# Kernel tuning notes

Hardware: AMD Instinct MI355X
Metric: run time of the kernel (lower is better)

## Reference

```python
import jax, jax.numpy as jnp
import numpy as np

N = 50000
E = 800000
D_IN = 128
H = 128
D_OUT = 64
BN_EPS = 1e-5


def setup_inputs() -> dict:
    key = jax.random.key(0)
    ks = jax.random.split(key, 20)

    def lin(k, fin, fout):
        kw, kb = jax.random.split(k)
        w = jax.random.normal(kw, (fin, fout), jnp.float32) / np.sqrt(fin)
        b = jnp.zeros((fout,), jnp.float32)
        return w, b

    def bn_params(k, d):
        kg, kb = jax.random.split(k)
        g = 1.0 + 0.1 * jax.random.normal(kg, (d,), jnp.float32)
        b = 0.1 * jax.random.normal(kb, (d,), jnp.float32)
        rm = 0.1 * jax.random.normal(jax.random.fold_in(k, 7), (d,), jnp.float32)
        rv = jnp.abs(1.0 + 0.1 * jax.random.normal(jax.random.fold_in(k, 9), (d,), jnp.float32))
        return g, b, rm, rv

    x = jax.random.normal(ks[0], (N, D_IN), jnp.float32)
    edge_index = jax.random.randint(ks[1], (2, E), 0, N, jnp.int64)
    ricci_curvature = jax.random.normal(ks[2], (E,), jnp.float32)

    W1, b1 = lin(ks[3], D_IN, H)
    Wc0, bc0 = lin(ks[4], H, H)          # convs[0]: hidden*1 -> hidden
    Wc1, bc1 = lin(ks[5], 2 * H, H)      # convs[1]: hidden*2 -> hidden
    Wout, bout = lin(ks[6], 3 * H, D_OUT)  # conv2: hidden*(L-1) -> out

    bn1_g, bn1_b, bn1_rm, bn1_rv = bn_params(ks[7], D_IN)
    bnc0_g, bnc0_b, bnc0_rm, bnc0_rv = bn_params(ks[8], H)
    bnc1_g, bnc1_b, bnc1_rm, bnc1_rv = bn_params(ks[9], 2 * H)
    bn2_g, bn2_b, bn2_rm, bn2_rv = bn_params(ks[10], 3 * H)

    return {
        "x": x, "edge_index": edge_index, "percent": 50,
        "ricci_curvature": ricci_curvature,
        "W1": W1, "b1": b1, "Wc0": Wc0, "bc0": bc0,
        "Wc1": Wc1, "bc1": bc1, "Wout": Wout, "bout": bout,
        "bn1_g": bn1_g, "bn1_b": bn1_b, "bn1_rm": bn1_rm, "bn1_rv": bn1_rv,
        "bnc0_g": bnc0_g, "bnc0_b": bnc0_b, "bnc0_rm": bnc0_rm, "bnc0_rv": bnc0_rv,
        "bnc1_g": bnc1_g, "bnc1_b": bnc1_b, "bnc1_rm": bnc1_rm, "bnc1_rv": bnc1_rv,
        "bn2_g": bn2_g, "bn2_b": bn2_b, "bn2_rm": bn2_rm, "bn2_rv": bn2_rv,
    }


def _bn_eval(h, g, b, rm, rv):
    # BatchNorm1d in eval mode: affine normalize with running stats.
    return (h - rm) * (g * jax.lax.rsqrt(rv + BN_EPS)) + b


def reference(x, edge_index, percent, ricci_curvature,
              W1, b1, Wc0, bc0, Wc1, bc1, Wout, bout,
              bn1_g, bn1_b, bn1_rm, bn1_rv,
              bnc0_g, bnc0_b, bnc0_rm, bnc0_rv,
              bnc1_g, bnc1_b, bnc1_rm, bnc1_rv,
              bn2_g, bn2_b, bn2_rm, bn2_rv):
    n = x.shape[0]
    # GCN normalization with self-loops (PyG GCNConv default), shared by all layers
    loops = jnp.arange(n, dtype=edge_index.dtype)
    row = jnp.concatenate([edge_index[0], loops])  # source
    col = jnp.concatenate([edge_index[1], loops])  # target
    deg = jax.ops.segment_sum(jnp.ones_like(col, dtype=x.dtype), col, num_segments=n)
    dinv = jax.lax.rsqrt(deg)  # deg >= 1 thanks to self loops
    norm = (dinv[row] * dinv[col])[:, None]  # [E+N, 1]

    def gcn(h, W, b):
        hw = h @ W                                   # transform first (PyG order)
        msg = hw[row] * norm                          # gather + scale per edge
        return jax.ops.segment_sum(msg, col, num_segments=n) + b

    # eval mode: no sampling / dynamic reweighting, dropout = identity
    h = _bn_eval(x, bn1_g, bn1_b, bn1_rm, bn1_rv)
    h = jax.nn.relu(gcn(h, W1, b1))
    r0 = h

    h = _bn_eval(h, bnc0_g, bnc0_b, bnc0_rm, bnc0_rv)
    h = jax.nn.relu(gcn(h, Wc0, bc0))
    r1 = h
    h = jnp.concatenate([r0, r1], axis=1)  # [N, 2H]

    h = _bn_eval(h, bnc1_g, bnc1_b, bnc1_rm, bnc1_rv)
    h = jax.nn.relu(gcn(h, Wc1, bc1))
    r2 = h
    h = jnp.concatenate([r0, r1, r2], axis=1)  # [N, 3H]

    h = _bn_eval(h, bn2_g, bn2_b, bn2_rm, bn2_rv)
    out = gcn(h, Wout, bout)
    return (out, r0, r1, r2)
```

## Files before the change

### kernel.cpp

```cpp
#include <hip/hip_runtime.h>
#include <hip/hip_bf16.h>
#include <stdint.h>

#define NN 50000
#define NE 800000

typedef unsigned short ushort8 __attribute__((ext_vector_type(8)));
typedef __bf16 bf16x8 __attribute__((ext_vector_type(8)));
typedef float f32x4 __attribute__((ext_vector_type(4)));

__device__ __forceinline__ float bf2f_bits(unsigned short u) {
  unsigned int x = ((unsigned int)u) << 16;
  float f;
  __builtin_memcpy(&f, &x, 4);
  return f;
}
__device__ __forceinline__ unsigned short f2bf_bits(float f) {
  unsigned int x;
  __builtin_memcpy(&x, &f, 4);
  unsigned int lsb = (x >> 16) & 1u;
  x += 0x7fffu + lsb;
  return (unsigned short)(x >> 16);
}
__device__ __forceinline__ float lo16(unsigned int v) { return bf2f_bits((unsigned short)v); }
__device__ __forceinline__ float hi16(unsigned int v) { return bf2f_bits((unsigned short)(v >> 16)); }
__device__ __forceinline__ float loadf(const void* base, size_t idx, int isbf) {
  if (isbf) return bf2f_bits(((const unsigned short*)base)[idx]);
  return ((const float*)base)[idx];
}

__global__ void k_sniff(const void* x, const void* ei, int* flags, int* cnt8) {
  int i = blockIdx.x * 256 + threadIdx.x;
  if (i < 8 * NN) cnt8[i] = 0;
  if (blockIdx.x != 0) return;
  __shared__ int badbf;
  __shared__ int zodd;
  int tid = threadIdx.x;
  if (tid == 0) { badbf = 0; zodd = 0; }
  __syncthreads();
  unsigned short u = ((const unsigned short*)x)[tid];
  float v = bf2f_bits(u);
  float av = fabsf(v);
  int ok = (av == 0.0f) || (av > 1e-8f && av < 1e8f);
  if (!ok) atomicAdd(&badbf, 1);
  int e32 = ((const int*)ei)[tid];
  if ((tid & 1) && e32 == 0) atomicAdd(&zodd, 1);
  __syncthreads();
  if (tid == 0) {
    flags[0] = (badbf <= 12) ? 1 : 0;
    flags[1] = (zodd >= 100) ? 1 : 0;
  }
}

__global__ void k_cvt_edges(const void* ei, int* erow, int* ecol, int* rank,
                            int* cnt8, const int* flags) {
  int e = blockIdx.x * 256 + threadIdx.x;
  if (e >= NE) return;
  unsigned int xcc;
  asm volatile("s_getreg_b32 %0, hwreg(HW_REG_XCC_ID)" : "=s"(xcc));
  xcc &= 7;
  int r, c;
  if (flags[1]) {
    const long long* p = (const long long*)ei;
    r = (int)p[e];
    c = (int)p[NE + e];
  } else {
    const int* p = (const int*)ei;
    r = p[e];
    c = p[NE + e];
  }
  erow[e] = r;
  ecol[e] = c;
  int rl = atomicAdd(&cnt8[xcc * NN + c], 1);
  rank[e] = rl | (int)(xcc << 27);
}

__global__ void k_cvt_xb(const void* x, unsigned short* xb, const int* flags) {
  if (flags[0]) return;
  int i4 = (blockIdx.x * 256 + threadIdx.x) * 4;
  if (i4 >= NN * 128) return;
  float4 v = *reinterpret_cast<const float4*>((const float*)x + i4);
  xb[i4 + 0] = f2bf_bits(v.x); xb[i4 + 1] = f2bf_bits(v.y);
  xb[i4 + 2] = f2bf_bits(v.z); xb[i4 + 3] = f2bf_bits(v.w);
}

__global__ void k_scan1(int* cnt8, int* indptr, int* bsum, float* dinv, int n) {
  __shared__ int sm[256];
  int tid = threadIdx.x;
  int i = blockIdx.x * 256 + tid;
  int v = 0;
  if (i < n) {
    int run = 0;
#pragma unroll
    for (int s = 0; s < 8; ++s) {
      int cs = cnt8[s * NN + i];
      cnt8[s * NN + i] = run;
      run += cs;
    }
    v = run;
    dinv[i] = rsqrtf((float)(v + 1));
  }
  sm[tid] = v;
  __syncthreads();
  for (int off = 1; off < 256; off <<= 1) {
    int t = (tid >= off) ? sm[tid - off] : 0;
    __syncthreads();
    sm[tid] += t;
    __syncthreads();
  }
  if (i < n) indptr[i] = sm[tid] - v;
  if (tid == 255) bsum[blockIdx.x] = sm[255];
}
__global__ void k_scan2(int* bsum, int nb) {
  __shared__ int sm[256];
  int tid = threadIdx.x;
  int v = (tid < nb) ? bsum[tid] : 0;
  sm[tid] = v;
  __syncthreads();
  for (int off = 1; off < 256; off <<= 1) {
    int t = (tid >= off) ? sm[tid - off] : 0;
    __syncthreads();
    sm[tid] += t;
    __syncthreads();
  }
  if (tid < nb) bsum[tid] = sm[tid] - v;
  if (tid == 0) bsum[nb] = sm[255];
}
__global__ void k_scan3(int* indptr, const int* bsum, int n, int nb) {
  int i = blockIdx.x * 256 + threadIdx.x;
  if (i < n) indptr[i] += bsum[i >> 8];
  else if (i == n) indptr[n] = bsum[nb];
}
__global__ void k_fill(const int* erow, const int* ecol, const int* rank,
                       const int* indptr, const int* cnt8, int* srcs) {
  int e = blockIdx.x * 256 + threadIdx.x;
  if (e >= NE) return;
  int c = ecol[e];
  int rk = rank[e];
  int sh = (unsigned int)rk >> 27;
  srcs[indptr[c] + cnt8[sh * NN + c] + (rk & 0x07FFFFFF)] = erow[e];
}

__global__ void k_prep_wt_all(
    const void* W1, const void* Wc0, const void* Wc1, const void* Wout,
    const void* g1, const void* g2, const void* g3, const void* g4,
    const void* rv1, const void* rv2, const void* rv3, const void* rv4,
    unsigned short* Wtb, const int* flags) {
  int idx = blockIdx.x * 256 + threadIdx.x;
  if (idx >= 90112) return;
  int isbf = flags[0];
  const void *W, *g, *rv;
  int K, NOUT, base;
  if (idx < 16384)      { W = W1;   g = g1; rv = rv1; K = 128; NOUT = 128; base = 0; }
  else if (idx < 32768) { W = Wc0;  g = g2; rv = rv2; K = 128; NOUT = 128; base = 16384; }
  else if (idx < 65536) { W = Wc1;  g = g3; rv = rv3; K = 256; NOUT = 128; base = 32768; }
  else                  { W = Wout; g = g4; rv = rv4; K = 384; NOUT = 64;  base = 65536; }
  int li = idx - base;
  int j = li / K, k = li % K;
  float s = loadf(g, k, isbf) * rsqrtf(loadf(rv, k, isbf) + 1e-5f);
  Wtb[idx] = f2bf_bits(s * loadf(W, (size_t)k * NOUT + j, isbf));
}
__global__ void k_prep_c_all(
    const void* W1, const void* Wc0, const void* Wc1, const void* Wout,
    const void* g1, const void* g2, const void* g3, const void* g4,
    const void* b1, const void* b2, const void* b3, const void* b4,
    const void* rm1, const void* rm2, const void* rm3, const void* rm4,
    const void* rv1, const void* rv2, const void* rv3, const void* rv4,
    float* cvec, const int* flags) {
  int jj = blockIdx.x;
  int lane = threadIdx.x;
  int isbf = flags[0];
  const void *W, *g, *bb, *rm, *rv;
  int K, NOUT, j;
  if (jj < 128)      { W = W1;   g = g1; bb = b1; rm = rm1; rv = rv1; K = 128; NOUT = 128; j = jj; }
  else if (jj < 256) { W = Wc0;  g = g2; bb = b2; rm = rm2; rv = rv2; K = 128; NOUT = 128; j = jj - 128; }
  else if (jj < 384) { W = Wc1;  g = g3; bb = b3; rm = rm3; rv = rv3; K = 256; NOUT = 128; j = jj - 256; }
  else               { W = Wout; g = g4; bb = b4; rm = rm4; rv = rv4; K = 384; NOUT = 64;  j = jj - 384; }
  float acc = 0.f;
  for (int k = lane; k < K; k += 64) {
    float s = loadf(g, k, isbf) * rsqrtf(loadf(rv, k, isbf) + 1e-5f);
    float t = loadf(bb, k, isbf) - loadf(rm, k, isbf) * s;
    acc += t * loadf(W, (size_t)k * NOUT + j, isbf);
  }
#pragma unroll
  for (int off = 32; off; off >>= 1) acc += __shfl_down(acc, off);
  if (lane == 0) cvec[jj] = acc;
}

template <int NOUT, int K>
__global__ __launch_bounds__(256) void k_gemm_mfma(
    const unsigned short* __restrict__ h0b, const unsigned short* __restrict__ h1b,
    const unsigned short* __restrict__ h2b,
    const unsigned short* __restrict__ h0d, const unsigned short* __restrict__ h1d,
    const unsigned short* __restrict__ h2d,
    const unsigned short* __restrict__ Wtb,
    const float* __restrict__ cvec, const float* __restrict__ dinv,
    unsigned short* __restrict__ hb, const int* __restrict__ flags) {
  constexpr int KS = K / 32;
  constexpr int NT = NOUT / 16;
  int isbf = flags[0];
  const unsigned short* h0 = (isbf && h0d) ? h0d : h0b;
  const unsigned short* h1 = (isbf && h1d) ? h1d : h1b;
  const unsigned short* h2 = (isbf && h2d) ? h2d : h2b;
  int tid = threadIdx.x;
  int wv = tid >> 6, lane = tid & 63;
  int row0 = blockIdx.x * 64 + wv * 16;
  int l15 = lane & 15;
  int kq = lane >> 4;
  int arow = row0 + l15;
  bool inb = arow < NN;

  bf16x8 afrag[KS];
#pragma unroll
  for (int ks = 0; ks < KS; ++ks) {
    int kg = ks * 32 + kq * 8;
    const unsigned short* src = (kg >> 7) == 0 ? h0 : ((kg >> 7) == 1 ? h1 : h2);
    ushort8 u = (ushort8)0;
    if (inb) u = *reinterpret_cast<const ushort8*>(src + (size_t)arow * 128 + (kg & 127));
    afrag[ks] = __builtin_bit_cast(bf16x8, u);
  }

  f32x4 acc[NT];
#pragma unroll
  for (int nt = 0; nt < NT; ++nt) acc[nt] = (f32x4)0.f;

#pragma unroll
  for (int nt = 0; nt < NT; ++nt) {
    const unsigned short* wrow = Wtb + (size_t)(nt * 16 + l15) * K + kq * 8;
#pragma unroll
    for (int ks = 0; ks < KS; ++ks) {
      ushort8 u = *reinterpret_cast<const ushort8*>(wrow + ks * 32);
      acc[nt] = __builtin_amdgcn_mfma_f32_16x16x32_bf16(
          afrag[ks], __builtin_bit_cast(bf16x8, u), acc[nt], 0, 0, 0);
    }
  }

  int orow0 = row0 + kq * 4;
  float dv[4];
  bool ob[4];
#pragma unroll
  for (int r = 0; r < 4; ++r) {
    int orow = orow0 + r;
    ob[r] = orow < NN;
    dv[r] = ob[r] ? dinv[orow] : 0.f;
  }
#pragma unroll
  for (int nt = 0; nt < NT; ++nt) {
    int col = nt * 16 + l15;
    float cv = cvec[col];
#pragma unroll
    for (int r = 0; r < 4; ++r) {
      if (ob[r])
        hb[(size_t)(orow0 + r) * NOUT + col] = f2bf_bits(dv[r] * (acc[nt][r] + cv));
    }
  }
}

template <bool RELU>
__global__ __launch_bounds__(256) void k_agg128(
    const unsigned short* __restrict__ hb, const int* __restrict__ indptr,
    const int* __restrict__ srcs, const float* __restrict__ dinv,
    const void* __restrict__ bias, void* __restrict__ dout, size_t region_off,
    unsigned short* __restrict__ rb, const int* __restrict__ flags) {
  int gw = __builtin_amdgcn_readfirstlane(blockIdx.x * 4 + (threadIdx.x >> 6));
  int lane = threadIdx.x & 63;
  if (gw >= NN) return;
  int isbf = flags[0];
  int e0 = indptr[gw], e1 = indptr[gw + 1];
  size_t co = (size_t)lane * 2;
  unsigned int sv = *reinterpret_cast<const unsigned int*>(hb + (size_t)gw * 128 + co);
  float a0 = lo16(sv), a1 = hi16(sv);
  float b0 = 0.f, b1 = 0.f, c0 = 0.f, c1 = 0.f, d0 = 0.f, d1 = 0.f;
  int e = e0;
  for (; e + 7 < e1; e += 8) {
    int s0 = srcs[e], s1 = srcs[e + 1], s2 = srcs[e + 2], s3 = srcs[e + 3];
    int s4 = srcs[e + 4], s5 = srcs[e + 5], s6 = srcs[e + 6], s7 = srcs[e + 7];
    unsigned int v0 = *reinterpret_cast<const unsigned int*>(hb + (size_t)s0 * 128 + co);
    unsigned int v1 = *reinterpret_cast<const unsigned int*>(hb + (size_t)s1 * 128 + co);
    unsigned int v2 = *reinterpret_cast<const unsigned int*>(hb + (size_t)s2 * 128 + co);
    unsigned int v3 = *reinterpret_cast<const unsigned int*>(hb + (size_t)s3 * 128 + co);
    unsigned int v4 = *reinterpret_cast<const unsigned int*>(hb + (size_t)s4 * 128 + co);
    unsigned int v5 = *reinterpret_cast<const unsigned int*>(hb + (size_t)s5 * 128 + co);
    unsigned int v6 = *reinterpret_cast<const unsigned int*>(hb + (size_t)s6 * 128 + co);
    unsigned int v7 = *reinterpret_cast<const unsigned int*>(hb + (size_t)s7 * 128 + co);
    a0 += lo16(v0); a1 += hi16(v0); b0 += lo16(v1); b1 += hi16(v1);
    c0 += lo16(v2); c1 += hi16(v2); d0 += lo16(v3); d1 += hi16(v3);
    a0 += lo16(v4); a1 += hi16(v4); b0 += lo16(v5); b1 += hi16(v5);
    c0 += lo16(v6); c1 += hi16(v6); d0 += lo16(v7); d1 += hi16(v7);
  }
  for (; e < e1; ++e) {
    int s0 = srcs[e];
    unsigned int v0 = *reinterpret_cast<const unsigned int*>(hb + (size_t)s0 * 128 + co);
    a0 += lo16(v0); a1 += hi16(v0);
  }
  float dv = dinv[gw];
  float o0 = dv * ((a0 + b0) + (c0 + d0)) + loadf(bias, co + 0, isbf);
  float o1 = dv * ((a1 + b1) + (c1 + d1)) + loadf(bias, co + 1, isbf);
  if (RELU) { o0 = fmaxf(o0, 0.f); o1 = fmaxf(o1, 0.f); }
  size_t eo = region_off + (size_t)gw * 128 + co;
  if (isbf) {
    unsigned int pk = (unsigned int)f2bf_bits(o0) | ((unsigned int)f2bf_bits(o1) << 16);
    *reinterpret_cast<unsigned int*>((unsigned short*)dout + eo) = pk;
  } else {
    float2 fo; fo.x = o0; fo.y = o1;
    *reinterpret_cast<float2*>((float*)dout + eo) = fo;
    unsigned int pk = (unsigned int)f2bf_bits(o0) | ((unsigned int)f2bf_bits(o1) << 16);
    *reinterpret_cast<unsigned int*>(rb + (size_t)gw * 128 + co) = pk;
  }
}

__global__ __launch_bounds__(256) void k_agg64out(
    const unsigned short* __restrict__ hb, const int* __restrict__ indptr,
    const int* __restrict__ srcs, const float* __restrict__ dinv,
    const void* __restrict__ bias, void* __restrict__ dout,
    const int* __restrict__ flags) {
  int gw = blockIdx.x * 8 + (threadIdx.x >> 5);
  int lane = threadIdx.x & 31;
  if (gw >= NN) return;
  int isbf = flags[0];
  int e0 = indptr[gw], e1 = indptr[gw + 1];
  int e = e0;
  size_t co = (size_t)lane * 2;
  unsigned int sv = *reinterpret_cast<const unsigned int*>(hb + (size_t)gw * 64 + co);
  float a0 = lo16(sv), a1 = hi16(sv);
  float b0 = 0.f, b1 = 0.f, c0 = 0.f, c1 = 0.f, d0 = 0.f, d1 = 0.f;
  for (; e + 3 < e1; e += 4) {
    int sa = srcs[e], sb = srcs[e + 1], sc = srcs[e + 2], sd = srcs[e + 3];
    unsigned int va = *reinterpret_cast<const unsigned int*>(hb + (size_t)sa * 64 + co);
    unsigned int vb = *reinterpret_cast<const unsigned int*>(hb + (size_t)sb * 64 + co);
    unsigned int vc = *reinterpret_cast<const unsigned int*>(hb + (size_t)sc * 64 + co);
    unsigned int vd = *reinterpret_cast<const unsigned int*>(hb + (size_t)sd * 64 + co);
    a0 += lo16(va); a1 += hi16(va); b0 += lo16(vb); b1 += hi16(vb);
    c0 += lo16(vc); c1 += hi16(vc); d0 += lo16(vd); d1 += hi16(vd);
  }
  for (; e < e1; ++e) {
    int sa = srcs[e];
    unsigned int va = *reinterpret_cast<const unsigned int*>(hb + (size_t)sa * 64 + co);
    a0 += lo16(va); a1 += hi16(va);
  }
  float dv = dinv[gw];
  float o0 = dv * ((a0 + b0) + (c0 + d0)) + loadf(bias, co + 0, isbf);
  float o1 = dv * ((a1 + b1) + (c1 + d1)) + loadf(bias, co + 1, isbf);
  size_t eo = (size_t)gw * 64 + co;
  if (isbf) {
    unsigned int pk = (unsigned int)f2bf_bits(o0) | ((unsigned int)f2bf_bits(o1) << 16);
    *reinterpret_cast<unsigned int*>((unsigned short*)dout + eo) = pk;
  } else {
    float2 fo; fo.x = o0; fo.y = o1;
    *reinterpret_cast<float2*>((float*)dout + eo) = fo;
  }
}

extern "C" void kernel_launch(void* const* d_in, const int* in_sizes, int n_in,
                              void* d_out, int out_size, void* d_ws, size_t ws_size,
                              hipStream_t stream) {
  const void* x    = d_in[0];
  const void* ei   = d_in[1];
  const void* W1   = d_in[4];
  const void* b1   = d_in[5];
  const void* Wc0  = d_in[6];
  const void* bc0  = d_in[7];
  const void* Wc1  = d_in[8];
  const void* bc1  = d_in[9];
  const void* Wout = d_in[10];
  const void* bout = d_in[11];
  const void *bn1g = d_in[12], *bn1b = d_in[13], *bn1rm = d_in[14], *bn1rv = d_in[15];
  const void *bc0g = d_in[16], *bc0b = d_in[17], *bc0rm = d_in[18], *bc0rv = d_in[19];
  const void *bc1g = d_in[20], *bc1b = d_in[21], *bc1rm = d_in[22], *bc1rv = d_in[23];
  const void *bn2g = d_in[24], *bn2b = d_in[25], *bn2rm = d_in[26], *bn2rv = d_in[27];
  (void)in_sizes; (void)n_in; (void)out_size; (void)ws_size;

  char* w = (char*)d_ws;
  auto carve = [&](size_t bytes) {
    char* p = w;
    w += (bytes + 255) & ~(size_t)255;
    return p;
  };
  int*   flags  = (int*)  carve(256);
  float* dinv   = (float*)carve(sizeof(float) * NN);
  int*   cnt8   = (int*)  carve(sizeof(int) * 8 * NN);
  int*   indptr = (int*)  carve(sizeof(int) * (NN + 1));
  int*   bsum   = (int*)  carve(sizeof(int) * 256);
  int*   erow   = (int*)  carve(sizeof(int) * NE);
  int*   ecol   = (int*)  carve(sizeof(int) * NE);
  int*   rank   = (int*)  carve(sizeof(int) * NE);
  int*   srcs   = (int*)  carve(sizeof(int) * NE);
  unsigned short* Wtb = (unsigned short*)carve(sizeof(short) * 90112);
  float* cvec   = (float*)carve(sizeof(float) * 448);
  unsigned short* xb  = (unsigned short*)carve(sizeof(short) * (size_t)NN * 128);
  unsigned short* hb  = (unsigned short*)carve(sizeof(short) * (size_t)NN * 128);
  unsigned short* rb0 = (unsigned short*)carve(sizeof(short) * (size_t)NN * 128);
  unsigned short* rb1 = (unsigned short*)carve(sizeof(short) * (size_t)NN * 128);
  unsigned short* rb2 = (unsigned short*)carve(sizeof(short) * (size_t)NN * 128);

  const int gN8 = (8 * NN + 255) / 256;
  const int gE = (NE + 255) / 256;
  const int nb = (NN + 255) / 256;
  const int gG = (NN + 63) / 64;
  const int gA2 = (NN + 3) / 4;
  const int gA1 = (NN + 7) / 8;

  k_sniff<<<gN8, 256, 0, stream>>>(x, ei, flags, cnt8);
  k_cvt_edges<<<gE, 256, 0, stream>>>(ei, erow, ecol, rank, cnt8, flags);
  k_cvt_xb<<<(NN * 128 / 4 + 255) / 256, 256, 0, stream>>>(x, xb, flags);
  k_scan1<<<nb, 256, 0, stream>>>(cnt8, indptr, bsum, dinv, NN);
  k_scan2<<<1, 256, 0, stream>>>(bsum, nb);
  k_scan3<<<(NN + 1 + 255) / 256, 256, 0, stream>>>(indptr, bsum, NN, nb);
  k_fill<<<gE, 256, 0, stream>>>(erow, ecol, rank, indptr, cnt8, srcs);
  k_prep_wt_all<<<(90112 + 255) / 256, 256, 0, stream>>>(
      W1, Wc0, Wc1, Wout, bn1g, bc0g, bc1g, bn2g, bn1rv, bc0rv, bc1rv, bn2rv, Wtb, flags);
  k_prep_c_all<<<448, 64, 0, stream>>>(
      W1, Wc0, Wc1, Wout, bn1g, bc0g, bc1g, bn2g, bn1b, bc0b, bc1b, bn2b,
      bn1rm, bc0rm, bc1rm, bn2rm, bn1rv, bc0rv, bc1rv, bn2rv, cvec, flags);

  const size_t offO  = 0;
  const size_t offR0 = (size_t)NN * 64;
  const size_t offR1 = offR0 + (size_t)NN * 128;
  const size_t offR2 = offR1 + (size_t)NN * 128;
  unsigned short* d0 = (unsigned short*)d_out;

  k_gemm_mfma<128, 128><<<gG, 256, 0, stream>>>(
      xb, nullptr, nullptr, (const unsigned short*)x, nullptr, nullptr,
      Wtb + 0, cvec + 0, dinv, hb, flags);
  k_agg128<true><<<gA2, 256, 0, stream>>>(hb, indptr, srcs, dinv, b1, d_out, offR0, rb0, flags);

  k_gemm_mfma<128, 128><<<gG, 256, 0, stream>>>(
      rb0, nullptr, nullptr, d0 + offR0, nullptr, nullptr, Wtb + 16384, cvec + 128, dinv, hb, flags);
  k_agg128<true><<<gA2, 256, 0, stream>>>(hb, indptr, srcs, dinv, bc0, d_out, offR1, rb1, flags);

  k_gemm_mfma<128, 256><<<gG, 256, 0, stream>>>(
      rb0, rb1, nullptr, d0 + offR0, d0 + offR1, nullptr, Wtb + 32768, cvec + 256, dinv, hb, flags);
  k_agg128<true><<<gA2, 256, 0, stream>>>(hb, indptr, srcs, dinv, bc1, d_out, offR2, rb2, flags);

  k_gemm_mfma<64, 384><<<gG, 256, 0, stream>>>(
      rb0, rb1, rb2, d0 + offR0, d0 + offR1, d0 + offR2, Wtb + 65536, cvec + 384, dinv, hb, flags);
  k_agg64out<<<gA1, 256, 0, stream>>>(hb, indptr, srcs, dinv, bout, d_out, flags);
}
```

Before: 333.5 us.

## Fuse preprocessing kernels and merge CSR fill with first GEMM launch

Merges edge counting, x-to-bf16 conversion and weight/bias prep into one launch. It replaces the three-kernel scan with a two-kernel scheme where each block reduces the preceding block sums itself. It also runs the CSR fill and the first MFMA GEMM as disjoint block ranges of one launch, rereading edge_index instead of keeping erow/ecol copies. The aim is to cut launch overhead and intermediate traffic, at the cost of branchy heterogeneous kernels and hardcoded grid constants.

```diff
diff --git a/kernel.cpp b/kernel.cpp
--- a/kernel.cpp
+++ b/kernel.cpp
@@ -4,6 +4,11 @@
 
 #define NN 50000
 #define NE 800000
+#define GE 3125
+#define GX 6250
+#define GW 352
+#define GC 112
+#define NB 196
 
 typedef unsigned short ushort8 __attribute__((ext_vector_type(8)));
 typedef __bf16 bf16x8 __attribute__((ext_vector_type(8)));
@@ -52,36 +57,77 @@
   }
 }
 
-__global__ void k_cvt_edges(const void* ei, int* erow, int* ecol, int* rank,
-                            int* cnt8, const int* flags) {
-  int e = blockIdx.x * 256 + threadIdx.x;
-  if (e >= NE) return;
-  unsigned int xcc;
-  asm volatile("s_getreg_b32 %0, hwreg(HW_REG_XCC_ID)" : "=s"(xcc));
-  xcc &= 7;
-  int r, c;
-  if (flags[1]) {
-    const long long* p = (const long long*)ei;
-    r = (int)p[e];
-    c = (int)p[NE + e];
-  } else {
-    const int* p = (const int*)ei;
-    r = p[e];
-    c = p[NE + e];
-  }
-  erow[e] = r;
-  ecol[e] = c;
-  int rl = atomicAdd(&cnt8[xcc * NN + c], 1);
-  rank[e] = rl | (int)(xcc << 27);
-}
-
-__global__ void k_cvt_xb(const void* x, unsigned short* xb, const int* flags) {
-  if (flags[0]) return;
-  int i4 = (blockIdx.x * 256 + threadIdx.x) * 4;
-  if (i4 >= NN * 128) return;
-  float4 v = *reinterpret_cast<const float4*>((const float*)x + i4);
-  xb[i4 + 0] = f2bf_bits(v.x); xb[i4 + 1] = f2bf_bits(v.y);
-  xb[i4 + 2] = f2bf_bits(v.z); xb[i4 + 3] = f2bf_bits(v.w);
+__global__ __launch_bounds__(256) void k_fuse_prep(
+    const void* ei, const void* x, unsigned short* xb, int* rank, int* cnt8,
+    const void* W1, const void* Wc0, const void* Wc1, const void* Wout,
+    const void* g1, const void* g2, const void* g3, const void* g4,
+    const void* b1, const void* b2, const void* b3, const void* b4,
+    const void* rm1, const void* rm2, const void* rm3, const void* rm4,
+    const void* rv1, const void* rv2, const void* rv3, const void* rv4,
+    unsigned short* Wtb, float* cvec, const int* flags) {
+  int bid = blockIdx.x;
+  int tid = threadIdx.x;
+  if (bid < GE) {
+    int e = bid * 256 + tid;
+    if (e >= NE) return;
+    unsigned int xcc;
+    asm volatile("s_getreg_b32 %0, hwreg(HW_REG_XCC_ID)" : "=s"(xcc));
+    xcc &= 7;
+    int c;
+    if (flags[1]) c = (int)((const long long*)ei)[NE + e];
+    else          c = ((const int*)ei)[NE + e];
+    int rl = atomicAdd(&cnt8[xcc * NN + c], 1);
+    rank[e] = rl | (int)(xcc << 27);
+    return;
+  }
+  bid -= GE;
+  if (bid < GX) {
+    if (flags[0]) return;
+    int i4 = (bid * 256 + tid) * 4;
+    if (i4 >= NN * 128) return;
+    float4 v = *reinterpret_cast<const float4*>((const float*)x + i4);
+    xb[i4 + 0] = f2bf_bits(v.x); xb[i4 + 1] = f2bf_bits(v.y);
+    xb[i4 + 2] = f2bf_bits(v.z); xb[i4 + 3] = f2bf_bits(v.w);
+    return;
+  }
+  bid -= GX;
+  int isbf = flags[0];
+  if (bid < GW) {
+    int idx = bid * 256 + tid;
+    if (idx >= 90112) return;
+    const void *W, *g, *rv;
+    int K, NOUT, base;
+    if (idx < 16384)      { W = W1;   g = g1; rv = rv1; K = 128; NOUT = 128; base = 0; }
+    else if (idx < 32768) { W = Wc0;  g = g2; rv = rv2; K = 128; NOUT = 128; base = 16384; }
+    else if (idx < 65536) { W = Wc1;  g = g3; rv = rv3; K = 256; NOUT = 128; base = 32768; }
+    else                  { W = Wout; g = g4; rv = rv4; K = 384; NOUT = 64;  base = 65536; }
+    int li = idx - base;
+    int j = li / K, k = li % K;
+    float s = loadf(g, k, isbf) * rsqrtf(loadf(rv, k, isbf) + 1e-5f);
+    Wtb[idx] = f2bf_bits(s * loadf(W, (size_t)k * NOUT + j, isbf));
+    return;
+  }
+  bid -= GW;
+  {
+    int jj = bid * 4 + (tid >> 6);
+    int lane = tid & 63;
+    if (jj >= 448) return;
+    const void *W, *g, *bb, *rm, *rv;
+    int K, NOUT, j;
+    if (jj < 128)      { W = W1;   g = g1; bb = b1; rm = rm1; rv = rv1; K = 128; NOUT = 128; j = jj; }
+    else if (jj < 256) { W = Wc0;  g = g2; bb = b2; rm = rm2; rv = rv2; K = 128; NOUT = 128; j = jj - 128; }
+    else if (jj < 384) { W = Wc1;  g = g3; bb = b3; rm = rm3; rv = rv3; K = 256; NOUT = 128; j = jj - 256; }
+    else               { W = Wout; g = g4; bb = b4; rm = rm4; rv = rv4; K = 384; NOUT = 64;  j = jj - 384; }
+    float acc = 0.f;
+    for (int k = lane; k < K; k += 64) {
+      float s = loadf(g, k, isbf) * rsqrtf(loadf(rv, k, isbf) + 1e-5f);
+      float t = loadf(bb, k, isbf) - loadf(rm, k, isbf) * s;
+      acc += t * loadf(W, (size_t)k * NOUT + j, isbf);
+    }
+#pragma unroll
+    for (int off = 32; off; off >>= 1) acc += __shfl_down(acc, off);
+    if (lane == 0) cvec[jj] = acc;
+  }
 }
 
 __global__ void k_scan1(int* cnt8, int* indptr, int* bsum, float* dinv, int n) {
@@ -111,80 +157,115 @@
   if (i < n) indptr[i] = sm[tid] - v;
   if (tid == 255) bsum[blockIdx.x] = sm[255];
 }
-__global__ void k_scan2(int* bsum, int nb) {
+
+__global__ void k_scan23(int* indptr, const int* bsum, int n, int nb) {
   __shared__ int sm[256];
+  int b = blockIdx.x;
   int tid = threadIdx.x;
-  int v = (tid < nb) ? bsum[tid] : 0;
-  sm[tid] = v;
+  sm[tid] = (tid < nb && tid < b) ? bsum[tid] : 0;
   __syncthreads();
-  for (int off = 1; off < 256; off <<= 1) {
-    int t = (tid >= off) ? sm[tid - off] : 0;
+  for (int off = 128; off; off >>= 1) {
+    if (tid < off) sm[tid] += sm[tid + off];
     __syncthreads();
-    sm[tid] += t;
-    __syncthreads();
-  }
-  if (tid < nb) bsum[tid] = sm[tid] - v;
-  if (tid == 0) bsum[nb] = sm[255];
-}
-__global__ void k_scan3(int* indptr, const int* bsum, int n, int nb) {
-  int i = blockIdx.x * 256 + threadIdx.x;
-  if (i < n) indptr[i] += bsum[i >> 8];
-  else if (i == n) indptr[n] = bsum[nb];
-}
-__global__ void k_fill(const int* erow, const int* ecol, const int* rank,
-                       const int* indptr, const int* cnt8, int* srcs) {
-  int e = blockIdx.x * 256 + threadIdx.x;
-  if (e >= NE) return;
-  int c = ecol[e];
-  int rk = rank[e];
-  int sh = (unsigned int)rk >> 27;
-  srcs[indptr[c] + cnt8[sh * NN + c] + (rk & 0x07FFFFFF)] = erow[e];
-}
-
-__global__ void k_prep_wt_all(
-    const void* W1, const void* Wc0, const void* Wc1, const void* Wout,
-    const void* g1, const void* g2, const void* g3, const void* g4,
-    const void* rv1, const void* rv2, const void* rv3, const void* rv4,
-    unsigned short* Wtb, const int* flags) {
-  int idx = blockIdx.x * 256 + threadIdx.x;
-  if (idx >= 90112) return;
-  int isbf = flags[0];
-  const void *W, *g, *rv;
-  int K, NOUT, base;
-  if (idx < 16384)      { W = W1;   g = g1; rv = rv1; K = 128; NOUT = 128; base = 0; }
-  else if (idx < 32768) { W = Wc0;  g = g2; rv = rv2; K = 128; NOUT = 128; base = 16384; }
-  else if (idx < 65536) { W = Wc1;  g = g3; rv = rv3; K = 256; NOUT = 128; base = 32768; }
-  else                  { W = Wout; g = g4; rv = rv4; K = 384; NOUT = 64;  base = 65536; }
-  int li = idx - base;
-  int j = li / K, k = li % K;
-  float s = loadf(g, k, isbf) * rsqrtf(loadf(rv, k, isbf) + 1e-5f);
-  Wtb[idx] = f2bf_bits(s * loadf(W, (size_t)k * NOUT + j, isbf));
-}
-__global__ void k_prep_c_all(
-    const void* W1, const void* Wc0, const void* Wc1, const void* Wout,
-    const void* g1, const void* g2, const void* g3, const void* g4,
-    const void* b1, const void* b2, const void* b3, const void* b4,
-    const void* rm1, const void* rm2, const void* rm3, const void* rm4,
-    const void* rv1, const void* rv2, const void* rv3, const void* rv4,
-    float* cvec, const int* flags) {
-  int jj = blockIdx.x;
-  int lane = threadIdx.x;
-  int isbf = flags[0];
-  const void *W, *g, *bb, *rm, *rv;
-  int K, NOUT, j;
-  if (jj < 128)      { W = W1;   g = g1; bb = b1; rm = rm1; rv = rv1; K = 128; NOUT = 128; j = jj; }
-  else if (jj < 256) { W = Wc0;  g = g2; bb = b2; rm = rm2; rv = rv2; K = 128; NOUT = 128; j = jj - 128; }
-  else if (jj < 384) { W = Wc1;  g = g3; bb = b3; rm = rm3; rv = rv3; K = 256; NOUT = 128; j = jj - 256; }
-  else               { W = Wout; g = g4; bb = b4; rm = rm4; rv = rv4; K = 384; NOUT = 64;  j = jj - 384; }
-  float acc = 0.f;
-  for (int k = lane; k < K; k += 64) {
-    float s = loadf(g, k, isbf) * rsqrtf(loadf(rv, k, isbf) + 1e-5f);
-    float t = loadf(bb, k, isbf) - loadf(rm, k, isbf) * s;
-    acc += t * loadf(W, (size_t)k * NOUT + j, isbf);
-  }
-#pragma unroll
-  for (int off = 32; off; off >>= 1) acc += __shfl_down(acc, off);
-  if (lane == 0) cvec[jj] = acc;
+  }
+  int S = sm[0];
+  int i = b * 256 + tid;
+  if (i < n) indptr[i] += S;
+  else if (i == n) indptr[n] = NE;
+}
+
+template <int NOUT, int K>
+__device__ __forceinline__ void gemm_body(
+    int bid,
+    const unsigned short* __restrict__ h0, const unsigned short* __restrict__ h1,
+    const unsigned short* __restrict__ h2,
+    const unsigned short* __restrict__ Wtb,
+    const float* __restrict__ cvec, const float* __restrict__ dinv,
+    unsigned short* __restrict__ hb) {
+  constexpr int KS = K / 32;
+  constexpr int NT = NOUT / 16;
+  int tid = threadIdx.x;
+  int wv = tid >> 6, lane = tid & 63;
+  int row0 = bid * 64 + wv * 16;
+  int l15 = lane & 15;
+  int kq = lane >> 4;
+  int arow = row0 + l15;
+  bool inb = arow < NN;
+
+  bf16x8 afrag[KS];
+#pragma unroll
+  for (int ks = 0; ks < KS; ++ks) {
+    int kg = ks * 32 + kq * 8;
+    const unsigned short* src = (kg >> 7) == 0 ? h0 : ((kg >> 7) == 1 ? h1 : h2);
+    ushort8 u = (ushort8)0;
+    if (inb) u = *reinterpret_cast<const ushort8*>(src + (size_t)arow * 128 + (kg & 127));
+    afrag[ks] = __builtin_bit_cast(bf16x8, u);
+  }
+
+  f32x4 acc[NT];
+#pragma unroll
+  for (int nt = 0; nt < NT; ++nt) acc[nt] = (f32x4)0.f;
+
+#pragma unroll
+  for (int nt = 0; nt < NT; ++nt) {
+    const unsigned short* wrow = Wtb + (size_t)(nt * 16 + l15) * K + kq * 8;
+#pragma unroll
+    for (int ks = 0; ks < KS; ++ks) {
+      ushort8 u = *reinterpret_cast<const ushort8*>(wrow + ks * 32);
+      acc[nt] = __builtin_amdgcn_mfma_f32_16x16x32_bf16(
+          afrag[ks], __builtin_bit_cast(bf16x8, u), acc[nt], 0, 0, 0);
+    }
+  }
+
+  int orow0 = row0 + kq * 4;
+  float dv[4];
+  bool ob[4];
+#pragma unroll
+  for (int r = 0; r < 4; ++r) {
+    int orow = orow0 + r;
+    ob[r] = orow < NN;
+    dv[r] = ob[r] ? dinv[orow] : 0.f;
+  }
+#pragma unroll
+  for (int nt = 0; nt < NT; ++nt) {
+    int col = nt * 16 + l15;
+    float cv = cvec[col];
+#pragma unroll
+    for (int r = 0; r < 4; ++r) {
+      if (ob[r])
+        hb[(size_t)(orow0 + r) * NOUT + col] = f2bf_bits(dv[r] * (acc[nt][r] + cv));
+    }
+  }
+}
+
+__global__ __launch_bounds__(256) void k_fill_gemm1(
+    const void* ei, const int* __restrict__ rank, const int* __restrict__ indptr,
+    const int* __restrict__ cnt8, int* __restrict__ srcs,
+    const unsigned short* __restrict__ h0b, const unsigned short* __restrict__ h0d,
+    const unsigned short* __restrict__ Wtb, const float* __restrict__ cvec,
+    const float* __restrict__ dinv, unsigned short* __restrict__ hb,
+    const int* __restrict__ flags) {
+  int bid = blockIdx.x;
+  if (bid < GE) {
+    int e = bid * 256 + threadIdx.x;
+    if (e >= NE) return;
+    int r, c;
+    if (flags[1]) {
+      const long long* p = (const long long*)ei;
+      r = (int)p[e];
+      c = (int)p[NE + e];
+    } else {
+      const int* p = (const int*)ei;
+      r = p[e];
+      c = p[NE + e];
+    }
+    int rk = rank[e];
+    int sh = (unsigned int)rk >> 27;
+    srcs[indptr[c] + cnt8[sh * NN + c] + (rk & 0x07FFFFFF)] = r;
+    return;
+  }
+  const unsigned short* h0 = (flags[0] && h0d) ? h0d : h0b;
+  gemm_body<128, 128>(bid - GE, h0, nullptr, nullptr, Wtb, cvec, dinv, hb);
 }
 
 template <int NOUT, int K>
@@ -196,64 +277,11 @@
     const unsigned short* __restrict__ Wtb,
     const float* __restrict__ cvec, const float* __restrict__ dinv,
     unsigned short* __restrict__ hb, const int* __restrict__ flags) {
-  constexpr int KS = K / 32;
-  constexpr int NT = NOUT / 16;
   int isbf = flags[0];
   const unsigned short* h0 = (isbf && h0d) ? h0d : h0b;
   const unsigned short* h1 = (isbf && h1d) ? h1d : h1b;
   const unsigned short* h2 = (isbf && h2d) ? h2d : h2b;
-  int tid = threadIdx.x;
-  int wv = tid >> 6, lane = tid & 63;
-  int row0 = blockIdx.x * 64 + wv * 16;
-  int l15 = lane & 15;
-  int kq = lane >> 4;
-  int arow = row0 + l15;
-  bool inb = arow < NN;
-
-  bf16x8 afrag[KS];
-#pragma unroll
-  for (int ks = 0; ks < KS; ++ks) {
-    int kg = ks * 32 + kq * 8;
-    const unsigned short* src = (kg >> 7) == 0 ? h0 : ((kg >> 7) == 1 ? h1 : h2);
-    ushort8 u = (ushort8)0;
-    if (inb) u = *reinterpret_cast<const ushort8*>(src + (size_t)arow * 128 + (kg & 127));
-    afrag[ks] = __builtin_bit_cast(bf16x8, u);
-  }
-
-  f32x4 acc[NT];
-#pragma unroll
-  for (int nt = 0; nt < NT; ++nt) acc[nt] = (f32x4)0.f;
-
-#pragma unroll
-  for (int nt = 0; nt < NT; ++nt) {
-    const unsigned short* wrow = Wtb + (size_t)(nt * 16 + l15) * K + kq * 8;
-#pragma unroll
-    for (int ks = 0; ks < KS; ++ks) {
-      ushort8 u = *reinterpret_cast<const ushort8*>(wrow + ks * 32);
-      acc[nt] = __builtin_amdgcn_mfma_f32_16x16x32_bf16(
-          afrag[ks], __builtin_bit_cast(bf16x8, u), acc[nt], 0, 0, 0);
-    }
-  }
-
-  int orow0 = row0 + kq * 4;
-  float dv[4];
-  bool ob[4];
-#pragma unroll
-  for (int r = 0; r < 4; ++r) {
-    int orow = orow0 + r;
-    ob[r] = orow < NN;
-    dv[r] = ob[r] ? dinv[orow] : 0.f;
-  }
-#pragma unroll
-  for (int nt = 0; nt < NT; ++nt) {
-    int col = nt * 16 + l15;
-    float cv = cvec[col];
-#pragma unroll
-    for (int r = 0; r < 4; ++r) {
-      if (ob[r])
-        hb[(size_t)(orow0 + r) * NOUT + col] = f2bf_bits(dv[r] * (acc[nt][r] + cv));
-    }
-  }
+  gemm_body<NOUT, K>(blockIdx.x, h0, h1, h2, Wtb, cvec, dinv, hb);
 }
 
 template <bool RELU>
@@ -381,8 +409,6 @@
   int*   cnt8   = (int*)  carve(sizeof(int) * 8 * NN);
   int*   indptr = (int*)  carve(sizeof(int) * (NN + 1));
   int*   bsum   = (int*)  carve(sizeof(int) * 256);
-  int*   erow   = (int*)  carve(sizeof(int) * NE);
-  int*   ecol   = (int*)  carve(sizeof(int) * NE);
   int*   rank   = (int*)  carve(sizeof(int) * NE);
   int*   srcs   = (int*)  carve(sizeof(int) * NE);
   unsigned short* Wtb = (unsigned short*)carve(sizeof(short) * 90112);
@@ -394,24 +420,18 @@
   unsigned short* rb2 = (unsigned short*)carve(sizeof(short) * (size_t)NN * 128);
 
   const int gN8 = (8 * NN + 255) / 256;
-  const int gE = (NE + 255) / 256;
-  const int nb = (NN + 255) / 256;
   const int gG = (NN + 63) / 64;
   const int gA2 = (NN + 3) / 4;
   const int gA1 = (NN + 7) / 8;
 
   k_sniff<<<gN8, 256, 0, stream>>>(x, ei, flags, cnt8);
-  k_cvt_edges<<<gE, 256, 0, stream>>>(ei, erow, ecol, rank, cnt8, flags);
-  k_cvt_xb<<<(NN * 128 / 4 + 255) / 256, 256, 0, stream>>>(x, xb, flags);
-  k_scan1<<<nb, 256, 0, stream>>>(cnt8, indptr, bsum, dinv, NN);
-  k_scan2<<<1, 256, 0, stream>>>(bsum, nb);
-  k_scan3<<<(NN + 1 + 255) / 256, 256, 0, stream>>>(indptr, bsum, NN, nb);
-  k_fill<<<gE, 256, 0, stream>>>(erow, ecol, rank, indptr, cnt8, srcs);
-  k_prep_wt_all<<<(90112 + 255) / 256, 256, 0, stream>>>(
-      W1, Wc0, Wc1, Wout, bn1g, bc0g, bc1g, bn2g, bn1rv, bc0rv, bc1rv, bn2rv, Wtb, flags);
-  k_prep_c_all<<<448, 64, 0, stream>>>(
-      W1, Wc0, Wc1, Wout, bn1g, bc0g, bc1g, bn2g, bn1b, bc0b, bc1b, bn2b,
-      bn1rm, bc0rm, bc1rm, bn2rm, bn1rv, bc0rv, bc1rv, bn2rv, cvec, flags);
+  k_fuse_prep<<<GE + GX + GW + GC, 256, 0, stream>>>(
+      ei, x, xb, rank, cnt8,
+      W1, Wc0, Wc1, Wout, bn1g, bc0g, bc1g, bn2g,
+      bn1b, bc0b, bc1b, bn2b, bn1rm, bc0rm, bc1rm, bn2rm,
+      bn1rv, bc0rv, bc1rv, bn2rv, Wtb, cvec, flags);
+  k_scan1<<<NB, 256, 0, stream>>>(cnt8, indptr, bsum, dinv, NN);
+  k_scan23<<<NB, 256, 0, stream>>>(indptr, bsum, NN, NB);
 
   const size_t offO  = 0;
   const size_t offR0 = (size_t)NN * 64;
@@ -419,9 +439,9 @@
   const size_t offR2 = offR1 + (size_t)NN * 128;
   unsigned short* d0 = (unsigned short*)d_out;
 
-  k_gemm_mfma<128, 128><<<gG, 256, 0, stream>>>(
-      xb, nullptr, nullptr, (const unsigned short*)x, nullptr, nullptr,
-      Wtb + 0, cvec + 0, dinv, hb, flags);
+  k_fill_gemm1<<<GE + gG, 256, 0, stream>>>(
+      ei, rank, indptr, cnt8, srcs,
+      xb, (const unsigned short*)x, Wtb + 0, cvec + 0, dinv, hb, flags);
   k_agg128<true><<<gA2, 256, 0, stream>>>(hb, indptr, srcs, dinv, b1, d_out, offR0, rb0, flags);
 
   k_gemm_mfma<128, 128><<<gG, 256, 0, stream>>>(
```

New measurement: 316.8 us (median of 2 runs). 5.0% less time.
